# Kernel optimization log

Measured on AMD Instinct MI355X. Metric: run time of the kernel, lower is better.

Reference implementation:

```python
import jax, jax.numpy as jnp
import numpy as np

EMBED_DIM = 1024
NUM_HEADS = 16
HEAD_DIM = EMBED_DIM // NUM_HEADS
SCALING = HEAD_DIM ** -0.5
NEG_FILL = -1e30


def setup_inputs() -> dict:
    key = jax.random.key(0)
    k1, k2, k3 = jax.random.split(key, 3)
    T, B, E = 2048, 4, EMBED_DIM
    query = jax.random.normal(k1, (T, B, E), dtype=jnp.float32)
    key_padding_mask = jnp.zeros((B, T), dtype=bool)  # 1 = padded key
    # xavier_uniform-like init
    lim_in = (6.0 / (3 * E + E)) ** 0.5
    in_proj_weight = jax.random.uniform(k2, (3 * E, E), minval=-lim_in, maxval=lim_in, dtype=jnp.float32)
    in_proj_bias = jnp.zeros((3 * E,), dtype=jnp.float32)
    lim_out = (6.0 / (E + E)) ** 0.5
    out_w = jax.random.uniform(k3, (E, E), minval=-lim_out, maxval=lim_out, dtype=jnp.float32)
    out_b = jnp.zeros((E,), dtype=jnp.float32)
    return {"query": query, "key_padding_mask": key_padding_mask,
            "in_proj_weight": in_proj_weight, "in_proj_bias": in_proj_bias,
            "out_w": out_w, "out_b": out_b}


def reference(query, key_padding_mask, in_proj_weight, in_proj_bias, out_w, out_b):
    T, B, E = query.shape
    H, D = NUM_HEADS, HEAD_DIM
    # fused in-projection (self-attention: qkv from same input)
    qkv = query @ in_proj_weight.T + in_proj_bias  # [T,B,3E]
    q, k, v = jnp.split(qkv, 3, axis=-1)
    q = q * SCALING
    q = q.reshape(T, B, H, D)
    k = k.reshape(T, B, H, D)
    v = v.reshape(T, B, H, D)
    # attention scores [B,H,T,S]
    scores = jnp.einsum('tbhd,sbhd->bhts', q, k)
    scores = jnp.where(key_padding_mask[:, None, None, :], NEG_FILL, scores)
    attn_w = jax.nn.softmax(scores, axis=-1)  # [B,H,T,S]
    # weighted sum of values -> [T,B,E]
    attn = jnp.einsum('bhts,sbhd->tbhd', attn_w, v).reshape(T, B, E)
    attn = attn @ out_w.T + out_b
    attn_w_avg = jnp.sum(attn_w, axis=1) / H  # [B,T,S]
    return attn, attn_w_avg
```

## Files before the change

### kernel.cpp

```cpp
#include <hip/hip_runtime.h>
#include <stdint.h>

#define QSCALE 0.18033688011112042f

typedef unsigned short u16;
typedef unsigned int u32;
typedef __attribute__((ext_vector_type(8))) __bf16 bf16x8;
typedef __attribute__((ext_vector_type(4))) float f32x4;
typedef __attribute__((ext_vector_type(16))) float f32x16;
typedef __attribute__((ext_vector_type(8))) u16 u16x8;
typedef __attribute__((ext_vector_type(4))) u32 u32x4;

__device__ __forceinline__ void gl_lds16(const void* g, void* l) {
  __builtin_amdgcn_global_load_lds(
      (const __attribute__((address_space(1))) void*)g,
      (__attribute__((address_space(3))) void*)l, 16, 0, 0);
}

__device__ __forceinline__ u16 f2bf(float f) {
  unsigned int u = __float_as_uint(f);
  u += 0x7FFFu + ((u >> 16) & 1u);
  return (u16)(u >> 16);
}

__device__ __forceinline__ u32 pk2(float a, float b) {
  return (u32)f2bf(a) | ((u32)f2bf(b) << 16);
}

extern "C" __global__ __launch_bounds__(256) void cvt_f32_bf16(
    const float* __restrict__ src, u16* __restrict__ dst, int n) {
  int i = (blockIdx.x * 256 + threadIdx.x) * 4;
  if (i >= n) return;
  float4 v = *(const float4*)(src + i);
  ushort4 o;
  o.x = f2bf(v.x); o.y = f2bf(v.y); o.z = f2bf(v.z); o.w = f2bf(v.w);
  *(ushort4*)(dst + i) = o;
}

extern "C" __global__ __launch_bounds__(256) void gemm_qkv(
    const u16* __restrict__ X, const u16* __restrict__ W,
    const float* __restrict__ bias,
    u16* __restrict__ qb, u16* __restrict__ kb, u16* __restrict__ vb) {
  const int tid = threadIdx.x;
  const int w = tid >> 6, lane = tid & 63;
  const int lg = lane >> 4, ll = lane & 15;
  const int wm = w >> 1, wn = w & 1;
  const int row0A = blockIdx.x * 128;
  const int row0B = blockIdx.y * 128;

  __shared__ __align__(16) u16 As[2][128 * 32];
  __shared__ __align__(16) u16 Bs[2][128 * 32];

  f32x4 acc[4][4] = {};

  const int r_st = tid >> 2;
  const int cb_st = (tid & 3) * 16;

#pragma unroll
  for (int it = 0; it < 2; ++it) {
    gl_lds16((const char*)X + ((size_t)(row0A + it * 64 + r_st) * 1024) * 2 + cb_st,
             (char*)&As[0][0] + it * 4096 + w * 1024);
    gl_lds16((const char*)W + ((size_t)(row0B + it * 64 + r_st) * 1024) * 2 + cb_st,
             (char*)&Bs[0][0] + it * 4096 + w * 1024);
  }

  for (int kt = 0; kt < 32; ++kt) {
    const int cur = kt & 1;
    asm volatile("s_waitcnt vmcnt(0)" ::: "memory");
    __syncthreads();
    if (kt + 1 < 32) {
      const int k0 = (kt + 1) * 32;
#pragma unroll
      for (int it = 0; it < 2; ++it) {
        gl_lds16((const char*)X + ((size_t)(row0A + it * 64 + r_st) * 1024 + k0) * 2 + cb_st,
                 (char*)&As[cur ^ 1][0] + it * 4096 + w * 1024);
        gl_lds16((const char*)W + ((size_t)(row0B + it * 64 + r_st) * 1024 + k0) * 2 + cb_st,
                 (char*)&Bs[cur ^ 1][0] + it * 4096 + w * 1024);
      }
    }
    const u16* Ab = &As[cur][0];
    const u16* Bb = &Bs[cur][0];
    const int kc = lg * 8;
    bf16x8 a[4], bfr[4];
#pragma unroll
    for (int i = 0; i < 4; ++i)
      a[i] = *(const bf16x8*)(Ab + (wm * 64 + i * 16 + ll) * 32 + kc);
#pragma unroll
    for (int j = 0; j < 4; ++j)
      bfr[j] = *(const bf16x8*)(Bb + (wn * 64 + j * 16 + ll) * 32 + kc);
#pragma unroll
    for (int i = 0; i < 4; ++i)
#pragma unroll
      for (int j = 0; j < 4; ++j)
        acc[i][j] = __builtin_amdgcn_mfma_f32_16x16x32_bf16(a[i], bfr[j], acc[i][j], 0, 0, 0);
  }

  const int which = row0B >> 10;
  u16* dst = which == 0 ? qb : (which == 1 ? kb : vb);
  const float scl = which == 0 ? QSCALE : 1.0f;
#pragma unroll
  for (int j = 0; j < 4; ++j) {
    const int n = row0B + wn * 64 + j * 16 + ll;
    const float bv = bias[n];
    const int n2 = n & 1023;
    const int hh = n2 >> 6, dd = n2 & 63;
#pragma unroll
    for (int i = 0; i < 4; ++i)
#pragma unroll
      for (int r = 0; r < 4; ++r) {
        const int m = row0A + wm * 64 + i * 16 + lg * 4 + r;
        const int tt = m >> 2, bb = m & 3;
        dst[((size_t)(bb * 16 + hh) * 2048 + tt) * 64 + dd] = f2bf((acc[i][j][r] + bv) * scl);
      }
  }
}

extern "C" __global__ __launch_bounds__(256) void transpose_v(
    const u16* __restrict__ v, u16* __restrict__ vt) {
  const int blk = blockIdx.x;
  const int bh = blk >> 5, tt = blk & 31;
  const int t0 = tt * 64;
  const int tid = threadIdx.x;
  __shared__ __align__(16) u16 tile[64][72];
  const u16* src = v + ((size_t)bh * 2048 + t0) * 64;
#pragma unroll
  for (int it = 0; it < 2; ++it) {
    const int r = it * 32 + (tid >> 3);
    const int c = (tid & 7) * 8;
    *(u16x8*)(&tile[r][c]) = *(const u16x8*)(src + (size_t)r * 64 + c);
  }
  __syncthreads();
  u16* dstb = vt + (size_t)bh * 64 * 2048 + t0;
#pragma unroll
  for (int it = 0; it < 2; ++it) {
    const int d = it * 32 + (tid >> 3);
    const int s = (tid & 7) * 8;
    u16x8 o;
#pragma unroll
    for (int jj = 0; jj < 8; ++jj) o[jj] = tile[s + jj][d];
    *(u16x8*)(dstb + (size_t)d * 2048 + s) = o;
  }
}

extern "C" __global__ __launch_bounds__(256, 4) void flash_fwd(
    const u16* __restrict__ q, const u16* __restrict__ k,
    const u16* __restrict__ vt, const unsigned char* __restrict__ mask,
    u16* __restrict__ attn_pre, float* __restrict__ stat_il) {
  const int blk = blockIdx.x;
  const int bh = blk >> 4, tt = blk & 15;
  const int b = bh >> 4, hd = bh & 15;
  const int t0 = tt * 128;
  const int tid = threadIdx.x, w = tid >> 6, lane = tid & 63;
  const int hl = lane >> 5;
  const int l31 = lane & 31;

  __shared__ __align__(16) u16 Ks[2][64 * 64];
  __shared__ __align__(16) u16 Vs[2][64 * 64];

  const int qrow = t0 + w * 32 + l31;
  const u16* qp = q + ((size_t)bh * 2048 + qrow) * 64 + hl * 8;
  bf16x8 qreg[4];
#pragma unroll
  for (int kg = 0; kg < 4; ++kg) qreg[kg] = *(const bf16x8*)(qp + kg * 16);

  f32x16 po[2] = {};
  float lsum = 0.f;

  const int slot_r = tid >> 3;
  const int slot_c8 = (tid & 7) ^ (slot_r & 7);
  const unsigned char* mrow = mask + b * 2048 + hl * 4;

#define STAGE_F(buf, s0_)                                                      \
  do {                                                                         \
    _Pragma("unroll") for (int it2 = 0; it2 < 2; ++it2) {                      \
      const int rr = it2 * 32 + slot_r;                                        \
      gl_lds16((const char*)k +                                                \
                   (((size_t)bh * 2048 + (s0_) + rr) * 64 + slot_c8 * 8) * 2,  \
               (char*)&Ks[buf][0] + it2 * 4096 + w * 1024);                    \
      gl_lds16((const char*)vt +                                               \
                   (((size_t)bh * 64 + rr) * 2048 + (s0_) + slot_c8 * 8) * 2,  \
               (char*)&Vs[buf][0] + it2 * 4096 + w * 1024);                    \
    }                                                                          \
  } while (0)

  STAGE_F(0, 0);
  asm volatile("s_waitcnt vmcnt(0)" ::: "memory");
  __syncthreads();

  for (int it = 0; it < 32; ++it) {
    const int s0 = it * 64;
    const int cur = it & 1;

    u32 mq[8];
#pragma unroll
    for (int kt = 0; kt < 2; ++kt)
#pragma unroll
      for (int j = 0; j < 4; ++j)
        mq[kt * 4 + j] = *(const u32*)(mrow + s0 + kt * 32 + j * 8);
    const u32 anym = mq[0] | mq[1] | mq[2] | mq[3] | mq[4] | mq[5] | mq[6] | mq[7];

    if (it + 1 < 32) STAGE_F(cur ^ 1, s0 + 64);

    const char* Kb = (const char*)&Ks[cur][0];
    const char* Vb = (const char*)&Vs[cur][0];

#pragma unroll
    for (int kt = 0; kt < 2; ++kt) {
      f32x16 z = {};
      const int key = kt * 32 + l31;
#pragma unroll
      for (int kg = 0; kg < 4; ++kg) {
        const bf16x8 kf = *(const bf16x8*)(
            Kb + key * 128 + ((((kg << 1) | hl) ^ (key & 7)) << 4));
        z = __builtin_amdgcn_mfma_f32_32x32x16_bf16(kf, qreg[kg], z, 0, 0, 0);
      }

      float ps[16];
#pragma unroll
      for (int r = 0; r < 16; ++r) ps[r] = __builtin_amdgcn_exp2f(z[r]);
      if (__any(anym != 0)) {
#pragma unroll
        for (int r = 0; r < 16; ++r)
          if ((mq[kt * 4 + (r >> 2)] >> ((r & 3) * 8)) & 0xFFu) ps[r] = 0.f;
      }
#pragma unroll
      for (int r = 0; r < 16; ++r) lsum += ps[r];

      u32 w8[8];
#pragma unroll
      for (int j = 0; j < 4; ++j) {
        w8[2 * j] = pk2(ps[4 * j], ps[4 * j + 1]);
        w8[2 * j + 1] = pk2(ps[4 * j + 2], ps[4 * j + 3]);
      }

#pragma unroll
      for (int f = 0; f < 2; ++f) {
        u32 d0 = w8[4 * f], d1 = w8[4 * f + 1];
        u32 s0w = w8[4 * f + 2], s1w = w8[4 * f + 3];
        asm volatile("v_permlane32_swap_b32 %0, %1" : "+v"(d0), "+v"(s0w));
        asm volatile("v_permlane32_swap_b32 %0, %1" : "+v"(d1), "+v"(s1w));
        const bf16x8 pa = __builtin_bit_cast(bf16x8, (u32x4){d0, d1, s0w, s1w});
        const int g = kt * 2 + f;
#pragma unroll
        for (int dt = 0; dt < 2; ++dt) {
          const int d = dt * 32 + l31;
          const bf16x8 vf = *(const bf16x8*)(
              Vb + d * 128 + ((((g << 1) | hl) ^ (d & 7)) << 4));
          po[dt] = __builtin_amdgcn_mfma_f32_32x32x16_bf16(pa, vf, po[dt], 0, 0, 0);
        }
      }
    }

    asm volatile("s_waitcnt vmcnt(0)" ::: "memory");
    __syncthreads();
  }

  lsum += __shfl_xor(lsum, 32, 64);
  const float linv = 1.0f / lsum;
  if (lane < 32)
    stat_il[(size_t)bh * 2048 + t0 + w * 32 + lane] = linv;

#pragma unroll
  for (int r = 0; r < 16; ++r) {
    const int qi = (r & 3) + 8 * (r >> 2) + 4 * hl;
    const float lv = __shfl(linv, qi, 64);
    const int trow = t0 + w * 32 + qi;
#pragma unroll
    for (int dt = 0; dt < 2; ++dt) {
      const int dd = dt * 32 + l31;
      attn_pre[((size_t)(trow * 4 + b)) * 1024 + hd * 64 + dd] =
          f2bf(po[dt][r] * lv);
    }
  }
#undef STAGE_F
}

extern "C" __global__ __launch_bounds__(256, 3) void wavg(
    const u16* __restrict__ q, const u16* __restrict__ k,
    const unsigned char* __restrict__ mask,
    const float* __restrict__ stat_il, float* __restrict__ wout) {
  const int blk = blockIdx.x;
  const int b = blk >> 9, tt = (blk >> 5) & 15, st = blk & 31;
  const int t0 = tt * 128, s0 = st * 64;
  const int tid = threadIdx.x, w = tid >> 6, lane = tid & 63;
  const int hl = lane >> 5;
  const int l31 = lane & 31;

  __shared__ __align__(16) u16 Qs[2][128 * 64];
  __shared__ __align__(16) u16 Ks2[2][64 * 64];

  const int slot_r8 = tid >> 3;
  const int slot_c8 = (tid & 7) ^ (slot_r8 & 7);

  u32 mq[8];
#pragma unroll
  for (int kt = 0; kt < 2; ++kt)
#pragma unroll
    for (int j = 0; j < 4; ++j)
      mq[kt * 4 + j] = *(const u32*)(mask + b * 2048 + s0 + kt * 32 + j * 8 + hl * 4);
  const u32 anym = mq[0] | mq[1] | mq[2] | mq[3] | mq[4] | mq[5] | mq[6] | mq[7];
  const bool domask = __any(anym != 0);

#define STAGE_W(buf, hh)                                                       \
  do {                                                                         \
    const size_t qo_ = (size_t)(b * 16 + (hh)) * 2048;                         \
    _Pragma("unroll") for (int i2 = 0; i2 < 4; ++i2) {                         \
      const int rr = i2 * 32 + slot_r8;                                        \
      gl_lds16((const char*)q + ((qo_ + t0 + rr) * 64 + slot_c8 * 8) * 2,      \
               (char*)&Qs[buf][0] + i2 * 4096 + w * 1024);                     \
    }                                                                          \
    _Pragma("unroll") for (int i2 = 0; i2 < 2; ++i2) {                         \
      const int rr = i2 * 32 + slot_r8;                                        \
      gl_lds16((const char*)k + ((qo_ + s0 + rr) * 64 + slot_c8 * 8) * 2,      \
               (char*)&Ks2[buf][0] + i2 * 4096 + w * 1024);                    \
    }                                                                          \
  } while (0)

  STAGE_W(0, 0);
  asm volatile("s_waitcnt vmcnt(0)" ::: "memory");
  __syncthreads();

  float accw[32] = {};
  for (int h = 0; h < 16; ++h) {
    const int cur = h & 1;
    const float ilh =
        stat_il[(size_t)(b * 16 + h) * 2048 + t0 + w * 32 + l31];

    if (h + 1 < 16) STAGE_W(cur ^ 1, h + 1);

    const char* Qb = (const char*)&Qs[cur][0];
    const char* Kb = (const char*)&Ks2[cur][0];

    const int qr = w * 32 + l31;
    bf16x8 qf[4];
#pragma unroll
    for (int kg = 0; kg < 4; ++kg)
      qf[kg] = *(const bf16x8*)(
          Qb + qr * 128 + ((((kg << 1) | hl) ^ (qr & 7)) << 4));

#pragma unroll
    for (int kt = 0; kt < 2; ++kt) {
      f32x16 z = {};
      const int key = kt * 32 + l31;
#pragma unroll
      for (int kg = 0; kg < 4; ++kg) {
        const bf16x8 kf = *(const bf16x8*)(
            Kb + key * 128 + ((((kg << 1) | hl) ^ (key & 7)) << 4));
        z = __builtin_amdgcn_mfma_f32_32x32x16_bf16(kf, qf[kg], z, 0, 0, 0);
      }
      float ps[16];
#pragma unroll
      for (int r = 0; r < 16; ++r) ps[r] = __builtin_amdgcn_exp2f(z[r]);
      if (domask) {
#pragma unroll
        for (int r = 0; r < 16; ++r)
          if ((mq[kt * 4 + (r >> 2)] >> ((r & 3) * 8)) & 0xFFu) ps[r] = 0.f;
      }
#pragma unroll
      for (int r = 0; r < 16; ++r)
        accw[kt * 16 + r] = fmaf(ps[r], ilh, accw[kt * 16 + r]);
    }

    asm volatile("s_waitcnt vmcnt(0)" ::: "memory");
    __syncthreads();
  }

  float* tb = ((float*)&Qs[0][0]) + w * 2048;
#pragma unroll
  for (int kt = 0; kt < 2; ++kt)
#pragma unroll
    for (int j = 0; j < 4; ++j) {
      f32x4 qd;
#pragma unroll
      for (int e = 0; e < 4; ++e) qd[e] = accw[kt * 16 + 4 * j + e] * 0.0625f;
      const int slot = kt * 8 + 2 * j + hl;
      *(f32x4*)(tb + l31 * 64 + ((slot ^ (l31 & 7)) << 2)) = qd;
    }
  __syncthreads();
#pragma unroll
  for (int j2 = 0; j2 < 8; ++j2) {
    const int row = j2 * 4 + (lane >> 4);
    const int slot = lane & 15;
    const f32x4 v = *(const f32x4*)(tb + row * 64 + ((slot ^ (row & 7)) << 2));
    *(f32x4*)(wout + ((size_t)b * 2048 + t0 + w * 32 + row) * 2048 + s0 +
              slot * 4) = v;
  }
#undef STAGE_W
}

extern "C" __global__ __launch_bounds__(256) void gemm_out(
    const u16* __restrict__ A, const u16* __restrict__ W,
    const float* __restrict__ bias, float* __restrict__ out) {
  const int tid = threadIdx.x;
  const int w = tid >> 6, lane = tid & 63;
  const int lg = lane >> 4, ll = lane & 15;
  const int wm = w >> 1, wn = w & 1;
  const int row0A = blockIdx.x * 128;
  const int row0B = blockIdx.y * 128;

  __shared__ __align__(16) u16 As[2][128 * 32];
  __shared__ __align__(16) u16 Bs[2][128 * 32];

  f32x4 acc[4][4] = {};
  const int r_st = tid >> 2;
  const int cb_st = (tid & 3) * 16;

#pragma unroll
  for (int it = 0; it < 2; ++it) {
    gl_lds16((const char*)A + ((size_t)(row0A + it * 64 + r_st) * 1024) * 2 + cb_st,
             (char*)&As[0][0] + it * 4096 + w * 1024);
    gl_lds16((const char*)W + ((size_t)(row0B + it * 64 + r_st) * 1024) * 2 + cb_st,
             (char*)&Bs[0][0] + it * 4096 + w * 1024);
  }

  for (int kt = 0; kt < 32; ++kt) {
    const int cur = kt & 1;
    asm volatile("s_waitcnt vmcnt(0)" ::: "memory");
    __syncthreads();
    if (kt + 1 < 32) {
      const int k0 = (kt + 1) * 32;
#pragma unroll
      for (int it = 0; it < 2; ++it) {
        gl_lds16((const char*)A + ((size_t)(row0A + it * 64 + r_st) * 1024 + k0) * 2 + cb_st,
                 (char*)&As[cur ^ 1][0] + it * 4096 + w * 1024);
        gl_lds16((const char*)W + ((size_t)(row0B + it * 64 + r_st) * 1024 + k0) * 2 + cb_st,
                 (char*)&Bs[cur ^ 1][0] + it * 4096 + w * 1024);
      }
    }
    const u16* Ab = &As[cur][0];
    const u16* Bb = &Bs[cur][0];
    const int kc = lg * 8;
    bf16x8 a[4], bfr[4];
#pragma unroll
    for (int i = 0; i < 4; ++i)
      a[i] = *(const bf16x8*)(Ab + (wm * 64 + i * 16 + ll) * 32 + kc);
#pragma unroll
    for (int j = 0; j < 4; ++j)
      bfr[j] = *(const bf16x8*)(Bb + (wn * 64 + j * 16 + ll) * 32 + kc);
#pragma unroll
    for (int i = 0; i < 4; ++i)
#pragma unroll
      for (int j = 0; j < 4; ++j)
        acc[i][j] = __builtin_amdgcn_mfma_f32_16x16x32_bf16(a[i], bfr[j], acc[i][j], 0, 0, 0);
  }

#pragma unroll
  for (int j = 0; j < 4; ++j) {
    const int n = row0B + wn * 64 + j * 16 + ll;
    const float bv = bias[n];
#pragma unroll
    for (int i = 0; i < 4; ++i)
#pragma unroll
      for (int r = 0; r < 4; ++r) {
        const int m = row0A + wm * 64 + i * 16 + lg * 4 + r;
        out[(size_t)m * 1024 + n] = acc[i][j][r] + bv;
      }
  }
}

extern "C" void kernel_launch(void* const* d_in, const int* in_sizes, int n_in,
                              void* d_out, int out_size, void* d_ws, size_t ws_size,
                              hipStream_t stream) {
  const float* query = (const float*)d_in[0];
  const unsigned char* mask = (const unsigned char*)d_in[1];
  const float* w_in = (const float*)d_in[2];
  const float* b_in = (const float*)d_in[3];
  const float* w_out = (const float*)d_in[4];
  const float* b_out = (const float*)d_in[5];

  float* out0 = (float*)d_out;
  float* outw = out0 + (size_t)8388608;

  char* ws = (char*)d_ws;
  u16* Xbf   = (u16*)(ws + 0);
  u16* Wqkv  = (u16*)(ws + 16777216);
  u16* Woutb = (u16*)(ws + 23068672);
  u16* qb    = (u16*)(ws + 25165824);
  u16* kb    = (u16*)(ws + 41943040);
  u16* vb    = (u16*)(ws + 58720256);
  u16* vtb   = (u16*)(ws + 75497472);
  u16* ap    = (u16*)(ws + 92274688);
  float* sil = (float*)(ws + 109051904);

  cvt_f32_bf16<<<8192, 256, 0, stream>>>(query, Xbf, 8388608);
  cvt_f32_bf16<<<3072, 256, 0, stream>>>(w_in, Wqkv, 3145728);
  cvt_f32_bf16<<<1024, 256, 0, stream>>>(w_out, Woutb, 1048576);
  gemm_qkv<<<dim3(64, 24), 256, 0, stream>>>(Xbf, Wqkv, b_in, qb, kb, vb);
  transpose_v<<<2048, 256, 0, stream>>>(vb, vtb);
  flash_fwd<<<1024, 256, 0, stream>>>(qb, kb, vtb, mask, ap, sil);
  wavg<<<2048, 256, 0, stream>>>(qb, kb, mask, sil, outw);
  gemm_out<<<dim3(64, 8), 256, 0, stream>>>(ap, Woutb, b_out, out0);
}
```

Baseline: 292.5 us.

## Fuse V transpose into QKV GEMM and triple-buffer flash attention loads

The QKV GEMM epilogue now writes V directly in transposed layout, so the separate transpose kernel and its extra round trip through memory go away. The flash kernel moves from double to triple buffering with one barrier per iteration and a partial vmcnt wait, so more K/V loads stay in flight. It also preloads the mask row into LDS and converts probabilities with the hardware packed bf16 instruction. Flash and wavg remap block indices so neighbouring blocks share data in cache. In exchange, the transposed V stores are strided and poorly coalesced, and flash_fwd's larger LDS footprint comes with a lower launch-bounds occupancy hint.

```diff
diff --git a/kernel.cpp b/kernel.cpp
--- a/kernel.cpp
+++ b/kernel.cpp
@@ -21,10 +21,6 @@
   unsigned int u = __float_as_uint(f);
   u += 0x7FFFu + ((u >> 16) & 1u);
   return (u16)(u >> 16);
-}
-
-__device__ __forceinline__ u32 pk2(float a, float b) {
-  return (u32)f2bf(a) | ((u32)f2bf(b) << 16);
 }
 
 extern "C" __global__ __launch_bounds__(256) void cvt_f32_bf16(
@@ -40,7 +36,7 @@
 extern "C" __global__ __launch_bounds__(256) void gemm_qkv(
     const u16* __restrict__ X, const u16* __restrict__ W,
     const float* __restrict__ bias,
-    u16* __restrict__ qb, u16* __restrict__ kb, u16* __restrict__ vb) {
+    u16* __restrict__ qb, u16* __restrict__ kb, u16* __restrict__ vtb) {
   const int tid = threadIdx.x;
   const int w = tid >> 6, lane = tid & 63;
   const int lg = lane >> 4, ll = lane & 15;
@@ -96,66 +92,60 @@
   }
 
   const int which = row0B >> 10;
-  u16* dst = which == 0 ? qb : (which == 1 ? kb : vb);
-  const float scl = which == 0 ? QSCALE : 1.0f;
-#pragma unroll
-  for (int j = 0; j < 4; ++j) {
-    const int n = row0B + wn * 64 + j * 16 + ll;
-    const float bv = bias[n];
-    const int n2 = n & 1023;
-    const int hh = n2 >> 6, dd = n2 & 63;
-#pragma unroll
-    for (int i = 0; i < 4; ++i)
-#pragma unroll
-      for (int r = 0; r < 4; ++r) {
-        const int m = row0A + wm * 64 + i * 16 + lg * 4 + r;
-        const int tt = m >> 2, bb = m & 3;
-        dst[((size_t)(bb * 16 + hh) * 2048 + tt) * 64 + dd] = f2bf((acc[i][j][r] + bv) * scl);
-      }
-  }
-}
-
-extern "C" __global__ __launch_bounds__(256) void transpose_v(
-    const u16* __restrict__ v, u16* __restrict__ vt) {
-  const int blk = blockIdx.x;
-  const int bh = blk >> 5, tt = blk & 31;
-  const int t0 = tt * 64;
-  const int tid = threadIdx.x;
-  __shared__ __align__(16) u16 tile[64][72];
-  const u16* src = v + ((size_t)bh * 2048 + t0) * 64;
-#pragma unroll
-  for (int it = 0; it < 2; ++it) {
-    const int r = it * 32 + (tid >> 3);
-    const int c = (tid & 7) * 8;
-    *(u16x8*)(&tile[r][c]) = *(const u16x8*)(src + (size_t)r * 64 + c);
-  }
-  __syncthreads();
-  u16* dstb = vt + (size_t)bh * 64 * 2048 + t0;
-#pragma unroll
-  for (int it = 0; it < 2; ++it) {
-    const int d = it * 32 + (tid >> 3);
-    const int s = (tid & 7) * 8;
-    u16x8 o;
-#pragma unroll
-    for (int jj = 0; jj < 8; ++jj) o[jj] = tile[s + jj][d];
-    *(u16x8*)(dstb + (size_t)d * 2048 + s) = o;
-  }
-}
-
-extern "C" __global__ __launch_bounds__(256, 4) void flash_fwd(
+  if (which == 2) {
+#pragma unroll
+    for (int j = 0; j < 4; ++j) {
+      const int n = row0B + wn * 64 + j * 16 + ll;
+      const float bv = bias[n];
+      const int n2 = n & 1023;
+      const int hh = n2 >> 6, dd = n2 & 63;
+#pragma unroll
+      for (int i = 0; i < 4; ++i)
+#pragma unroll
+        for (int r = 0; r < 4; ++r) {
+          const int m = row0A + wm * 64 + i * 16 + lg * 4 + r;
+          const int tt = m >> 2, bb = m & 3;
+          vtb[(((size_t)(bb * 16 + hh)) * 64 + dd) * 2048 + tt] =
+              f2bf(acc[i][j][r] + bv);
+        }
+    }
+  } else {
+    u16* dst = which == 0 ? qb : kb;
+    const float scl = which == 0 ? QSCALE : 1.0f;
+#pragma unroll
+    for (int j = 0; j < 4; ++j) {
+      const int n = row0B + wn * 64 + j * 16 + ll;
+      const float bv = bias[n];
+      const int n2 = n & 1023;
+      const int hh = n2 >> 6, dd = n2 & 63;
+#pragma unroll
+      for (int i = 0; i < 4; ++i)
+#pragma unroll
+        for (int r = 0; r < 4; ++r) {
+          const int m = row0A + wm * 64 + i * 16 + lg * 4 + r;
+          const int tt = m >> 2, bb = m & 3;
+          dst[((size_t)(bb * 16 + hh) * 2048 + tt) * 64 + dd] =
+              f2bf((acc[i][j][r] + bv) * scl);
+        }
+    }
+  }
+}
+
+extern "C" __global__ __launch_bounds__(256, 3) void flash_fwd(
     const u16* __restrict__ q, const u16* __restrict__ k,
     const u16* __restrict__ vt, const unsigned char* __restrict__ mask,
     u16* __restrict__ attn_pre, float* __restrict__ stat_il) {
-  const int blk = blockIdx.x;
-  const int bh = blk >> 4, tt = blk & 15;
+  const int lb = ((blockIdx.x & 7) << 7) + (blockIdx.x >> 3);
+  const int bh = lb >> 4, tt = lb & 15;
   const int b = bh >> 4, hd = bh & 15;
   const int t0 = tt * 128;
   const int tid = threadIdx.x, w = tid >> 6, lane = tid & 63;
   const int hl = lane >> 5;
   const int l31 = lane & 31;
 
-  __shared__ __align__(16) u16 Ks[2][64 * 64];
-  __shared__ __align__(16) u16 Vs[2][64 * 64];
+  __shared__ __align__(16) u16 Ks[3][64 * 64];
+  __shared__ __align__(16) u16 Vs[3][64 * 64];
+  __shared__ __align__(16) unsigned char Ms[2048];
 
   const int qrow = t0 + w * 32 + l31;
   const u16* qp = q + ((size_t)bh * 2048 + qrow) * 64 + hl * 8;
@@ -168,9 +158,8 @@
 
   const int slot_r = tid >> 3;
   const int slot_c8 = (tid & 7) ^ (slot_r & 7);
-  const unsigned char* mrow = mask + b * 2048 + hl * 4;
-
-#define STAGE_F(buf, s0_)                                                      \
+
+#define STAGE3(buf, s0_)                                                       \
   do {                                                                         \
     _Pragma("unroll") for (int it2 = 0; it2 < 2; ++it2) {                      \
       const int rr = it2 * 32 + slot_r;                                        \
@@ -183,26 +172,34 @@
     }                                                                          \
   } while (0)
 
-  STAGE_F(0, 0);
-  asm volatile("s_waitcnt vmcnt(0)" ::: "memory");
-  __syncthreads();
-
-  for (int it = 0; it < 32; ++it) {
-    const int s0 = it * 64;
-    const int cur = it & 1;
-
-    u32 mq[8];
-#pragma unroll
-    for (int kt = 0; kt < 2; ++kt)
-#pragma unroll
-      for (int j = 0; j < 4; ++j)
-        mq[kt * 4 + j] = *(const u32*)(mrow + s0 + kt * 32 + j * 8);
-    const u32 anym = mq[0] | mq[1] | mq[2] | mq[3] | mq[4] | mq[5] | mq[6] | mq[7];
-
-    if (it + 1 < 32) STAGE_F(cur ^ 1, s0 + 64);
-
+  if (w < 2)
+    gl_lds16((const char*)mask + b * 2048 + w * 1024 + lane * 16,
+             (char*)Ms + w * 1024);
+  STAGE3(0, 0);
+  STAGE3(1, 64);
+
+  for (int t = 0; t < 32; ++t) {
+    if (t < 31) {
+      asm volatile("s_waitcnt vmcnt(4)" ::: "memory");
+    } else {
+      asm volatile("s_waitcnt vmcnt(0)" ::: "memory");
+    }
+    __builtin_amdgcn_s_barrier();
+    if (t + 2 < 32) STAGE3((t + 2) % 3, (t + 2) * 64);
+
+    const int s0 = t * 64;
+    const int cur = t % 3;
     const char* Kb = (const char*)&Ks[cur][0];
     const char* Vb = (const char*)&Vs[cur][0];
+
+    u32 mq[8];
+#pragma unroll
+    for (int kt = 0; kt < 2; ++kt)
+#pragma unroll
+      for (int j = 0; j < 4; ++j)
+        mq[kt * 4 + j] =
+            *(const u32*)(Ms + s0 + kt * 32 + j * 8 + hl * 4);
+    const u32 anym = mq[0] | mq[1] | mq[2] | mq[3] | mq[4] | mq[5] | mq[6] | mq[7];
 
 #pragma unroll
     for (int kt = 0; kt < 2; ++kt) {
@@ -229,8 +226,10 @@
       u32 w8[8];
 #pragma unroll
       for (int j = 0; j < 4; ++j) {
-        w8[2 * j] = pk2(ps[4 * j], ps[4 * j + 1]);
-        w8[2 * j + 1] = pk2(ps[4 * j + 2], ps[4 * j + 3]);
+        asm("v_cvt_pk_bf16_f32 %0, %1, %2"
+            : "=v"(w8[2 * j]) : "v"(ps[4 * j]), "v"(ps[4 * j + 1]));
+        asm("v_cvt_pk_bf16_f32 %0, %1, %2"
+            : "=v"(w8[2 * j + 1]) : "v"(ps[4 * j + 2]), "v"(ps[4 * j + 3]));
       }
 
 #pragma unroll
@@ -250,9 +249,6 @@
         }
       }
     }
-
-    asm volatile("s_waitcnt vmcnt(0)" ::: "memory");
-    __syncthreads();
   }
 
   lsum += __shfl_xor(lsum, 32, 64);
@@ -272,15 +268,15 @@
           f2bf(po[dt][r] * lv);
     }
   }
-#undef STAGE_F
+#undef STAGE3
 }
 
 extern "C" __global__ __launch_bounds__(256, 3) void wavg(
     const u16* __restrict__ q, const u16* __restrict__ k,
     const unsigned char* __restrict__ mask,
     const float* __restrict__ stat_il, float* __restrict__ wout) {
-  const int blk = blockIdx.x;
-  const int b = blk >> 9, tt = (blk >> 5) & 15, st = blk & 31;
+  const int lb = ((blockIdx.x & 7) << 8) + (blockIdx.x >> 3);
+  const int b = lb >> 9, tt = (lb >> 5) & 15, st = lb & 31;
   const int t0 = tt * 128, s0 = st * 64;
   const int tid = threadIdx.x, w = tid >> 6, lane = tid & 63;
   const int hl = lane >> 5;
@@ -477,7 +473,6 @@
   u16* Woutb = (u16*)(ws + 23068672);
   u16* qb    = (u16*)(ws + 25165824);
   u16* kb    = (u16*)(ws + 41943040);
-  u16* vb    = (u16*)(ws + 58720256);
   u16* vtb   = (u16*)(ws + 75497472);
   u16* ap    = (u16*)(ws + 92274688);
   float* sil = (float*)(ws + 109051904);
@@ -485,8 +480,7 @@
   cvt_f32_bf16<<<8192, 256, 0, stream>>>(query, Xbf, 8388608);
   cvt_f32_bf16<<<3072, 256, 0, stream>>>(w_in, Wqkv, 3145728);
   cvt_f32_bf16<<<1024, 256, 0, stream>>>(w_out, Woutb, 1048576);
-  gemm_qkv<<<dim3(64, 24), 256, 0, stream>>>(Xbf, Wqkv, b_in, qb, kb, vb);
-  transpose_v<<<2048, 256, 0, stream>>>(vb, vtb);
+  gemm_qkv<<<dim3(64, 24), 256, 0, stream>>>(Xbf, Wqkv, b_in, qb, kb, vtb);
   flash_fwd<<<1024, 256, 0, stream>>>(qb, kb, vtb, mask, ap, sil);
   wavg<<<2048, 256, 0, stream>>>(qb, kb, mask, sil, outw);
   gemm_out<<<dim3(64, 8), 256, 0, stream>>>(ap, Woutb, b_out, out0);
```

Measured after the change: 305.6 us. 4.5% more time.
